# Optimization experiments

Hardware: AMD Instinct MI355X
Metric: run time of the kernel (lower is better)

## Reference

```python
import jax, jax.numpy as jnp
import numpy as np

DIM = 1024
HEADS = 16
DIM_HEAD = 64
NB_FEATURES = 266
EPS = 1e-4


def _gaussian_orthogonal_random_matrix(nb_rows, nb_cols, seed=0):
    # Blocks of orthogonal rows (QR of gaussian), rows rescaled by gaussian row norms (scaling=0).
    rng = np.random.default_rng(seed)
    blocks = []
    full, rem = divmod(nb_rows, nb_cols)
    for _ in range(full):
        g = rng.standard_normal((nb_cols, nb_cols))
        q, _ = np.linalg.qr(g)
        blocks.append(q.T)
    if rem > 0:
        g = rng.standard_normal((nb_cols, nb_cols))
        q, _ = np.linalg.qr(g)
        blocks.append(q.T[:rem])
    mat = np.concatenate(blocks, axis=0)
    multiplier = np.linalg.norm(rng.standard_normal((nb_rows, nb_cols)), axis=1)
    return (multiplier[:, None] * mat).astype(np.float32)


def _softmax_kernel(data, proj, is_query):
    # data: [b,h,n,d], proj: [m,d]
    d = data.shape[-1]
    data_normalizer = d ** -0.25
    ratio = proj.shape[0] ** -0.5
    data_dash = jnp.einsum('bhnd,md->bhnm', data * data_normalizer, proj)
    diag = 0.5 * (data_normalizer ** 2) * jnp.sum(data * data, axis=-1, keepdims=True)
    if is_query:
        m = jax.lax.stop_gradient(jnp.max(data_dash, axis=-1, keepdims=True))
    else:
        m = jax.lax.stop_gradient(jnp.max(data_dash, axis=(-1, -2), keepdims=True))
    return ratio * (jnp.exp(data_dash - diag - m) + EPS)


def _linear_attention(q, k, v):
    # q,k: [b,h,n,m], v: [b,h,n,e]
    k_cumsum = jnp.sum(k, axis=-2)                                   # [b,h,m]
    D_inv = 1.0 / jnp.einsum('bhnm,bhm->bhn', q, k_cumsum)           # [b,h,n]
    context = jnp.einsum('bhnm,bhne->bhme', k, v)                    # [b,h,m,e]
    return jnp.einsum('bhme,bhnm,bhn->bhne', context, q, D_inv)      # [b,h,n,e]


def setup_inputs() -> dict:
    key = jax.random.key(0)
    k1, k2, k3, k4, k5 = jax.random.split(key, 5)
    B, N = 2, 4096
    inner = HEADS * DIM_HEAD
    s = DIM ** -0.5
    return {
        'x': jax.random.normal(k1, (B, N, DIM), dtype=jnp.float32),
        'Wq': jax.random.normal(k2, (inner, DIM), dtype=jnp.float32) * s,
        'Wk': jax.random.normal(k3, (inner, DIM), dtype=jnp.float32) * s,
        'Wv': jax.random.normal(k4, (inner, DIM), dtype=jnp.float32) * s,
        'Wo': jax.random.normal(k5, (DIM, inner), dtype=jnp.float32) * s,
        'bo': jnp.zeros((DIM,), dtype=jnp.float32),
        'proj': jnp.asarray(_gaussian_orthogonal_random_matrix(NB_FEATURES, DIM_HEAD)),
    }


def reference(x, Wq, Wk, Wv, Wo, bo, proj):
    b, n, _ = x.shape
    def split_heads(t):
        return t.reshape(b, n, HEADS, DIM_HEAD).transpose(0, 2, 1, 3)  # [b,h,n,d]
    q = split_heads(x @ Wq.T)
    k = split_heads(x @ Wk.T)
    v = split_heads(x @ Wv.T)
    qp = _softmax_kernel(q, proj, is_query=True)
    kp = _softmax_kernel(k, proj, is_query=False)
    out = _linear_attention(qp, kp, v)                                # [b,h,n,d]
    out = out.transpose(0, 2, 1, 3).reshape(b, n, HEADS * DIM_HEAD)
    return out @ Wo.T + bo
```

## Files before the change

kernel.cpp:

```cpp
#include <hip/hip_runtime.h>
#include <hip/hip_bf16.h>
#include <hip/hip_fp16.h>


#define B_   2
#define N_   4096
#define H_   16
#define M_   266
#define MP_  288
#define DIM_ 1024
#define RT_  8192
#define BH_  32
#define LKN  40
#define LSB  296
#define NCH  16
#define KS_  8

typedef __attribute__((ext_vector_type(8))) short s8v;
typedef __attribute__((ext_vector_type(4))) float f4v;

__device__ __forceinline__ ushort f2bu(float x){ __hip_bfloat16 h = __float2bfloat16(x); return *(ushort*)&h; }

constexpr float NORMC  = 0.35355339059327379f;
constexpr float RATIOC = 0.06131393f;
constexpr float DIAGC  = 0.0625f;
constexpr float EPSC   = 1e-4f;

__device__ __forceinline__ unsigned encf(float x){
    unsigned b = __float_as_uint(x);
    return (b & 0x80000000u) ? ~b : (b | 0x80000000u);
}
__device__ __forceinline__ float decf(unsigned u){
    unsigned b = (u & 0x80000000u) ? (u ^ 0x80000000u) : ~u;
    return __uint_as_float(b);
}

__device__ __forceinline__ void stf(float* p, float v){ *p = v; }
__device__ __forceinline__ void stf(__hip_bfloat16* p, float v){ *p = __float2bfloat16(v); }

__device__ __forceinline__ void gl_lds16(const ushort* g, ushort* l){
    __builtin_amdgcn_global_load_lds(
        (const __attribute__((address_space(1))) unsigned int*)(const unsigned int*)g,
        (__attribute__((address_space(3))) unsigned int*)(unsigned int*)l,
        16, 0, 0);
}

__global__ void cast_x(const float* __restrict__ s, ushort* __restrict__ d){
    const int i = (blockIdx.x * 256 + threadIdx.x) * 8;
    const float4 a = *(const float4*)&s[i];
    const float4 b = *(const float4*)&s[i + 4];
    ushort4 lo, hi;
    lo.x = f2bu(a.x); lo.y = f2bu(a.y); lo.z = f2bu(a.z); lo.w = f2bu(a.w);
    hi.x = f2bu(b.x); hi.y = f2bu(b.y); hi.z = f2bu(b.z); hi.w = f2bu(b.w);
    *(ushort4*)&d[i]     = lo;
    *(ushort4*)&d[i + 4] = hi;
}

__global__ void cast_w(const float* s0, const float* s1, const float* s2, const float* s3,
                       ushort* d0, ushort* d1, ushort* d2, ushort* d3){
    const float* s; ushort* d;
    switch (blockIdx.y) {
        case 0: s = s0; d = d0; break;
        case 1: s = s1; d = d1; break;
        case 2: s = s2; d = d2; break;
        default: s = s3; d = d3; break;
    }
    const int i = (blockIdx.x * 256 + threadIdx.x) * 8;
    const float4 a = *(const float4*)&s[i];
    const float4 b = *(const float4*)&s[i + 4];
    ushort4 lo, hi;
    lo.x = f2bu(a.x); lo.y = f2bu(a.y); lo.z = f2bu(a.z); lo.w = f2bu(a.w);
    hi.x = f2bu(b.x); hi.y = f2bu(b.y); hi.z = f2bu(b.z); hi.w = f2bu(b.w);
    *(ushort4*)&d[i]     = lo;
    *(ushort4*)&d[i + 4] = hi;
}

__global__ void cast_proj(const float* __restrict__ p, ushort* __restrict__ pb){
    const int i = blockIdx.x * 256 + threadIdx.x;
    if (i >= MP_ * 64) return;
    const int m = i >> 6, dc = i & 63;
    pb[i] = f2bu((m < M_) ? NORMC * p[m * 64 + dc] : 0.f);
}

template<bool DIAG, bool BIAS, typename TC>
__launch_bounds__(256)
__global__ void gemm128(const ushort* __restrict__ A, const ushort* __restrict__ Bw,
                        const float* __restrict__ bias, TC* __restrict__ C,
                        float* __restrict__ diag)
{
    __shared__ ushort As[128 * 32];
    __shared__ ushort Bs[128 * 32];

    const int tid  = threadIdx.x;
    const int lane = tid & 63, wave = tid >> 6;
    const int col  = lane & 15, quad = lane >> 4;
    const int wm   = (wave & 1) * 64, wn = (wave >> 1) * 64;
    const int r0   = blockIdx.y * 128, c0 = blockIdx.x * 128;

    const int f0 = tid * 8;
    const int row0 = f0 >> 5, kc0 = f0 & 31;
    const size_t aoff0 = (size_t)(r0 + row0) * DIM_ + kc0;
    const size_t aoff1 = (size_t)(r0 + 64 + row0) * DIM_ + kc0;
    const size_t boff0 = (size_t)(c0 + row0) * DIM_ + kc0;
    const size_t boff1 = (size_t)(c0 + 64 + row0) * DIM_ + kc0;
    ushort* asb0 = &As[wave * 512];
    ushort* asb1 = &As[2048 + wave * 512];
    ushort* bsb0 = &Bs[wave * 512];
    ushort* bsb1 = &Bs[2048 + wave * 512];

    f4v acc[4][4];
    #pragma unroll
    for (int i = 0; i < 4; ++i)
        #pragma unroll
        for (int j = 0; j < 4; ++j) acc[i][j] = (f4v){0.f, 0.f, 0.f, 0.f};

    for (int kk = 0; kk < DIM_; kk += 32) {
        gl_lds16(&A[aoff0 + kk],  asb0);
        gl_lds16(&A[aoff1 + kk],  asb1);
        gl_lds16(&Bw[boff0 + kk], bsb0);
        gl_lds16(&Bw[boff1 + kk], bsb1);
        __syncthreads();
        s8v af[4], bf[4];
        #pragma unroll
        for (int i = 0; i < 4; ++i)
            af[i] = *(const s8v*)&As[(wm + i * 16 + col) * 32 + quad * 8];
        #pragma unroll
        for (int j = 0; j < 4; ++j)
            bf[j] = *(const s8v*)&Bs[(wn + j * 16 + col) * 32 + quad * 8];
        #pragma unroll
        for (int i = 0; i < 4; ++i)
            #pragma unroll
            for (int j = 0; j < 4; ++j)
                acc[i][j] = __builtin_amdgcn_mfma_f32_16x16x32_bf16(af[i], bf[j], acc[i][j], 0, 0, 0);
        __syncthreads();
    }

    float bb[4] = {0.f, 0.f, 0.f, 0.f};
    if (BIAS) {
        #pragma unroll
        for (int j = 0; j < 4; ++j) bb[j] = bias[c0 + wn + j * 16 + col];
    }
    #pragma unroll
    for (int i = 0; i < 4; ++i) {
        #pragma unroll
        for (int r = 0; r < 4; ++r) {
            const size_t grow = (size_t)(r0 + wm + i * 16 + quad * 4 + r);
            #pragma unroll
            for (int j = 0; j < 4; ++j)
                stf(&C[grow * DIM_ + c0 + wn + j * 16 + col], acc[i][j][r] + bb[j]);
        }
    }
    if (DIAG) {
        const int hglob = (c0 + wn) >> 6;
        #pragma unroll
        for (int i = 0; i < 4; ++i) {
            #pragma unroll
            for (int r = 0; r < 4; ++r) {
                float s = 0.f;
                #pragma unroll
                for (int j = 0; j < 4; ++j) s += acc[i][j][r] * acc[i][j][r];
                s += __shfl_xor(s, 1); s += __shfl_xor(s, 2);
                s += __shfl_xor(s, 4); s += __shfl_xor(s, 8);
                if (col == 0)
                    diag[(size_t)(r0 + wm + i * 16 + quad * 4 + r) * H_ + hglob] = DIAGC * s;
            }
        }
    }
}

__launch_bounds__(256)
__global__ void gemm128_qkv(const ushort* __restrict__ A, const ushort* __restrict__ Bw,
                            ushort* __restrict__ Q, ushort* __restrict__ K,
                            ushort* __restrict__ V,
                            float* __restrict__ diagQ, float* __restrict__ diagK)
{
    __shared__ ushort As[128 * 32];
    __shared__ ushort Bs[128 * 32];

    const int tid  = threadIdx.x;
    const int lane = tid & 63, wave = tid >> 6;
    const int col  = lane & 15, quad = lane >> 4;
    const int wm   = (wave & 1) * 64, wn = (wave >> 1) * 64;
    const int r0   = blockIdx.y * 128, c0 = blockIdx.x * 128;

    const int f0 = tid * 8;
    const int row0 = f0 >> 5, kc0 = f0 & 31;
    const size_t aoff0 = (size_t)(r0 + row0) * DIM_ + kc0;
    const size_t aoff1 = (size_t)(r0 + 64 + row0) * DIM_ + kc0;
    const size_t boff0 = (size_t)(c0 + row0) * DIM_ + kc0;
    const size_t boff1 = (size_t)(c0 + 64 + row0) * DIM_ + kc0;
    ushort* asb0 = &As[wave * 512];
    ushort* asb1 = &As[2048 + wave * 512];
    ushort* bsb0 = &Bs[wave * 512];
    ushort* bsb1 = &Bs[2048 + wave * 512];

    f4v acc[4][4];
    #pragma unroll
    for (int i = 0; i < 4; ++i)
        #pragma unroll
        for (int j = 0; j < 4; ++j) acc[i][j] = (f4v){0.f, 0.f, 0.f, 0.f};

    for (int kk = 0; kk < DIM_; kk += 32) {
        gl_lds16(&A[aoff0 + kk],  asb0);
        gl_lds16(&A[aoff1 + kk],  asb1);
        gl_lds16(&Bw[boff0 + kk], bsb0);
        gl_lds16(&Bw[boff1 + kk], bsb1);
        __syncthreads();
        s8v af[4], bf[4];
        #pragma unroll
        for (int i = 0; i < 4; ++i)
            af[i] = *(const s8v*)&As[(wm + i * 16 + col) * 32 + quad * 8];
        #pragma unroll
        for (int j = 0; j < 4; ++j)
            bf[j] = *(const s8v*)&Bs[(wn + j * 16 + col) * 32 + quad * 8];
        #pragma unroll
        for (int i = 0; i < 4; ++i)
            #pragma unroll
            for (int j = 0; j < 4; ++j)
                acc[i][j] = __builtin_amdgcn_mfma_f32_16x16x32_bf16(af[i], bf[j], acc[i][j], 0, 0, 0);
        __syncthreads();
    }

    const int which = c0 >> 10;
    const int cc    = c0 & 1023;
    ushort* C = (which == 0) ? Q : ((which == 1) ? K : V);
    float* dptr = (which == 0) ? diagQ : ((which == 1) ? diagK : nullptr);

    #pragma unroll
    for (int i = 0; i < 4; ++i) {
        #pragma unroll
        for (int r = 0; r < 4; ++r) {
            const size_t grow = (size_t)(r0 + wm + i * 16 + quad * 4 + r);
            #pragma unroll
            for (int j = 0; j < 4; ++j)
                C[grow * DIM_ + cc + wn + j * 16 + col] = f2bu(acc[i][j][r]);
        }
    }
    if (dptr) {
        const int hglob = (cc + wn) >> 6;
        #pragma unroll
        for (int i = 0; i < 4; ++i) {
            #pragma unroll
            for (int r = 0; r < 4; ++r) {
                float s = 0.f;
                #pragma unroll
                for (int j = 0; j < 4; ++j) s += acc[i][j][r] * acc[i][j][r];
                s += __shfl_xor(s, 1); s += __shfl_xor(s, 2);
                s += __shfl_xor(s, 4); s += __shfl_xor(s, 8);
                if (col == 0)
                    dptr[(size_t)(r0 + wm + i * 16 + quad * 4 + r) * H_ + hglob] = DIAGC * s;
            }
        }
    }
}

__launch_bounds__(256)
__global__ void kmax_mfma(const ushort* __restrict__ Kb, const ushort* __restrict__ projb,
                          unsigned* __restrict__ kmaxb)
{
    __shared__ ushort Pl[MP_ * 64];
    __shared__ float wmx[4];
    const int tid  = threadIdx.x;
    const int lane = tid & 63, wave = tid >> 6;
    const int col  = lane & 15, quad = lane >> 4;
    const int bh   = blockIdx.y, b = bh >> 4, h = bh & 15;

    const size_t arowB = ((size_t)(b * N_ + blockIdx.x * 256 + wave * 16 + col)) * DIM_ + h * 64 + quad * 8;
    s8v aP0 = *(const s8v*)&Kb[arowB];
    s8v aP1 = *(const s8v*)&Kb[arowB + 32];

    for (int i = tid; i < MP_ * 8; i += 256) {
        const int m = i >> 3, c = i & 7;
        *(uint4*)&Pl[m * 64 + ((c ^ (m & 7)) << 3)] = *(const uint4*)&projb[m * 64 + (c << 3)];
    }
    __syncthreads();

    const int sw0 = (quad ^ (col & 7)) << 3;
    const int sw1 = ((quad | 4) ^ (col & 7)) << 3;

    float mx = -3.4e38f;
    #pragma unroll
    for (int ni = 0; ni < 4; ++ni) {
        const s8v af0 = aP0, af1 = aP1;
        if (ni < 3) {
            aP0 = *(const s8v*)&Kb[arowB + (size_t)(ni + 1) * 64 * DIM_];
            aP1 = *(const s8v*)&Kb[arowB + (size_t)(ni + 1) * 64 * DIM_ + 32];
        }
        #pragma unroll
        for (int t = 0; t < 17; ++t) {
            const s8v bf0 = *(const s8v*)&Pl[(t * 16 + col) * 64 + sw0];
            const s8v bf1 = *(const s8v*)&Pl[(t * 16 + col) * 64 + sw1];
            f4v a = (f4v){0.f, 0.f, 0.f, 0.f};
            a = __builtin_amdgcn_mfma_f32_16x16x32_bf16(af0, bf0, a, 0, 0, 0);
            a = __builtin_amdgcn_mfma_f32_16x16x32_bf16(af1, bf1, a, 0, 0, 0);
            if (t * 16 + col < M_) {
                #pragma unroll
                for (int r = 0; r < 4; ++r) mx = fmaxf(mx, a[r]);
            }
        }
    }
    #pragma unroll
    for (int o = 32; o > 0; o >>= 1) mx = fmaxf(mx, __shfl_xor(mx, o));
    if (lane == 0) wmx[wave] = mx;
    __syncthreads();
    if (tid == 0)
        atomicMax(&kmaxb[bh], encf(fmaxf(fmaxf(wmx[0], wmx[1]), fmaxf(wmx[2], wmx[3]))));
}

__launch_bounds__(256)
__global__ void kctx_mfma(const ushort* __restrict__ Kb, const ushort* __restrict__ Vb,
                          const ushort* __restrict__ projb,
                          const float* __restrict__ diagK, const unsigned* __restrict__ kmaxb,
                          float* __restrict__ ctxp, float* __restrict__ kcsp)
{
    __shared__ ushort Pl[MP_ * 64];
    __shared__ ushort Kp[MP_ * LKN];
    __shared__ ushort Vt[64 * LKN];
    __shared__ float kred[2][MP_];

    const int tid  = threadIdx.x;
    const int lane = tid & 63, wave = tid >> 6;
    const int col  = lane & 15, quad = lane >> 4;
    const int bh   = blockIdx.y, b = bh >> 4, h = bh & 15;
    const int n0   = blockIdx.x * (N_ / NCH);
    const float kmax = decf(kmaxb[bh]);
    const int rowblk = wave >> 1;
    const int t0 = (wave & 1) * 9;

    const int nst = tid & 31, est = (tid >> 5) * 8;
    s8v vvP = *(const s8v*)&Vb[((size_t)(b * N_ + n0 + nst)) * DIM_ + h * 64 + est];
    const size_t arow0 = ((size_t)(b * N_ + n0 + rowblk * 16 + col)) * DIM_ + h * 64 + quad * 8;
    s8v afP0 = *(const s8v*)&Kb[arow0];
    s8v afP1 = *(const s8v*)&Kb[arow0 + 32];
    float dgrP[4];
    #pragma unroll
    for (int r = 0; r < 4; ++r)
        dgrP[r] = diagK[((size_t)(b * N_ + n0 + rowblk * 16 + quad * 4 + r)) * H_ + h];

    for (int i = tid; i < MP_ * 8; i += 256) {
        const int m = i >> 3, c = i & 7;
        *(uint4*)&Pl[m * 64 + ((c ^ (m & 7)) << 3)] = *(const uint4*)&projb[m * 64 + (c << 3)];
    }
    const int sw0 = (quad ^ (col & 7)) << 3;
    const int sw1 = ((quad | 4) ^ (col & 7)) << 3;

    f4v facc[18];
    #pragma unroll
    for (int t = 0; t < 18; ++t) facc[t] = (f4v){0.f, 0.f, 0.f, 0.f};
    float kcsa[9] = {};

    __syncthreads();

    for (int ks = 0; ks < KS_; ++ks) {
        const s8v vv = vvP, af0 = afP0, af1 = afP1;
        float dgr[4];
        #pragma unroll
        for (int r = 0; r < 4; ++r) dgr[r] = dgrP[r];

        #pragma unroll
        for (int j = 0; j < 8; ++j) Vt[(est + j) * LKN + nst] = ((const ushort*)&vv)[j];

        for (int t = t0; t < t0 + 9; ++t) {
            const s8v bf0 = *(const s8v*)&Pl[(t * 16 + col) * 64 + sw0];
            const s8v bf1 = *(const s8v*)&Pl[(t * 16 + col) * 64 + sw1];
            f4v a = (f4v){0.f, 0.f, 0.f, 0.f};
            a = __builtin_amdgcn_mfma_f32_16x16x32_bf16(af0, bf0, a, 0, 0, 0);
            a = __builtin_amdgcn_mfma_f32_16x16x32_bf16(af1, bf1, a, 0, 0, 0);
            const int m = t * 16 + col;
            float kp[4];
            #pragma unroll
            for (int r = 0; r < 4; ++r) {
                float v = 0.f;
                if (m < M_) v = RATIOC * (__expf(a[r] - dgr[r] - kmax) + EPSC);
                kp[r] = v;
            }
            kcsa[t - t0] += kp[0] + kp[1] + kp[2] + kp[3];
            ushort4 pk;
            pk.x = f2bu(kp[0]); pk.y = f2bu(kp[1]); pk.z = f2bu(kp[2]); pk.w = f2bu(kp[3]);
            *(ushort4*)&Kp[m * LKN + rowblk * 16 + quad * 4] = pk;
        }

        if (ks + 1 < KS_) {
            const int nb1 = n0 + (ks + 1) * 32;
            vvP  = *(const s8v*)&Vb[((size_t)(b * N_ + nb1 + nst)) * DIM_ + h * 64 + est];
            const size_t arow1 = ((size_t)(b * N_ + nb1 + rowblk * 16 + col)) * DIM_ + h * 64 + quad * 8;
            afP0 = *(const s8v*)&Kb[arow1];
            afP1 = *(const s8v*)&Kb[arow1 + 32];
            #pragma unroll
            for (int r = 0; r < 4; ++r)
                dgrP[r] = diagK[((size_t)(b * N_ + nb1 + rowblk * 16 + quad * 4 + r)) * H_ + h];
        }
        __syncthreads();
        const s8v bfe = *(const s8v*)&Vt[(wave * 16 + col) * LKN + quad * 8];
        #pragma unroll
        for (int t = 0; t < 18; ++t) {
            const s8v am = *(const s8v*)&Kp[(t * 16 + col) * LKN + quad * 8];
            facc[t] = __builtin_amdgcn_mfma_f32_16x16x32_bf16(am, bfe, facc[t], 0, 0, 0);
        }
        __syncthreads();
    }

    const size_t pbase = ((size_t)bh * NCH + blockIdx.x) * (MP_ * 64);
    #pragma unroll
    for (int t = 0; t < 18; ++t) {
        #pragma unroll
        for (int r = 0; r < 4; ++r)
            ctxp[pbase + (size_t)(t * 16 + quad * 4 + r) * 64 + wave * 16 + col] = facc[t][r];
    }
    for (int t = t0; t < t0 + 9; ++t) {
        float s = kcsa[t - t0];
        s += __shfl_xor(s, 16);
        s += __shfl_xor(s, 32);
        if (quad == 0) kred[rowblk][t * 16 + col] = s;
    }
    __syncthreads();
    for (int i = tid; i < MP_; i += 256)
        kcsp[((size_t)bh * NCH + blockIdx.x) * MP_ + i] = kred[0][i] + kred[1][i];
}

__launch_bounds__(256)
__global__ void ctx_reduce(const float* __restrict__ ctxp, const float* __restrict__ kcsp,
                           ushort* __restrict__ ctxT, float* __restrict__ kcs)
{
    const int bh = blockIdx.y, tid = threadIdx.x;
    const int base = blockIdx.x * (MP_ * 64 / 8);
    const size_t cb = (size_t)bh * NCH * (MP_ * 64);
    #pragma unroll
    for (int u = 0; u < 9; ++u) {
        const int flat = base + u * 256 + tid;
        float s = 0.f;
        #pragma unroll
        for (int c = 0; c < NCH; ++c) s += ctxp[cb + (size_t)c * (MP_ * 64) + flat];
        const int m = flat >> 6, e = flat & 63;
        ctxT[((size_t)bh * 64 + e) * MP_ + m] = f2bu(s);
    }
    if (blockIdx.x == 0) {
        for (int i = tid; i < MP_; i += 256) {
            float s = 0.f;
            #pragma unroll
            for (int c = 0; c < NCH; ++c) s += kcsp[((size_t)bh * NCH + c) * MP_ + i];
            kcs[(size_t)bh * MP_ + i] = s;
        }
    }
}

__launch_bounds__(256)
__global__ void qdashout(const ushort* __restrict__ Qb, const ushort* __restrict__ projb,
                         const float* __restrict__ diagQ, const float* __restrict__ kcs,
                         const ushort* __restrict__ ctxT, ushort* __restrict__ Ab)
{
    __shared__ ushort SB[64 * LSB];
    __shared__ float kcl[MP_];
    __shared__ float dinv[64];

    const int tid  = threadIdx.x;
    const int lane = tid & 63, wave = tid >> 6;
    const int col  = lane & 15, quad = lane >> 4;
    const int bh   = blockIdx.y, b = bh >> 4, h = bh & 15;
    const int n0   = blockIdx.x * 64;

    const size_t arow = ((size_t)(b * N_ + n0 + wave * 16 + col)) * DIM_ + h * 64 + quad * 8;
    const s8v af0 = *(const s8v*)&Qb[arow];
    const s8v af1 = *(const s8v*)&Qb[arow + 32];
    float dgr[4];
    #pragma unroll
    for (int r = 0; r < 4; ++r)
        dgr[r] = diagQ[((size_t)(b * N_ + n0 + wave * 16 + quad * 4 + r)) * H_ + h];

    for (int i = tid; i < MP_ * 8; i += 256) {
        const int m = i >> 3, c = i & 7;
        *(uint4*)&SB[m * 64 + ((c ^ (m & 7)) << 3)] = *(const uint4*)&projb[m * 64 + (c << 3)];
    }
    for (int i = tid; i < MP_; i += 256) kcl[i] = kcs[(size_t)bh * MP_ + i];
    __syncthreads();

    const int sw0 = (quad ^ (col & 7)) << 3;
    const int sw1 = ((quad | 4) ^ (col & 7)) << 3;

    f4v acc[17];
    #pragma unroll
    for (int t = 0; t < 17; ++t) {
        const s8v bf0 = *(const s8v*)&SB[(t * 16 + col) * 64 + sw0];
        const s8v bf1 = *(const s8v*)&SB[(t * 16 + col) * 64 + sw1];
        f4v a = (f4v){0.f, 0.f, 0.f, 0.f};
        a = __builtin_amdgcn_mfma_f32_16x16x32_bf16(af0, bf0, a, 0, 0, 0);
        a = __builtin_amdgcn_mfma_f32_16x16x32_bf16(af1, bf1, a, 0, 0, 0);
        acc[t] = a;
    }

    float rmx[4];
    #pragma unroll
    for (int r = 0; r < 4; ++r) {
        float mx = -3.4e38f;
        #pragma unroll
        for (int t = 0; t < 16; ++t) mx = fmaxf(mx, acc[t][r]);
        if (col < 10) mx = fmaxf(mx, acc[16][r]);
        mx = fmaxf(mx, __shfl_xor(mx, 1));
        mx = fmaxf(mx, __shfl_xor(mx, 2));
        mx = fmaxf(mx, __shfl_xor(mx, 4));
        mx = fmaxf(mx, __shfl_xor(mx, 8));
        rmx[r] = mx;
    }

    float den[4] = {0.f, 0.f, 0.f, 0.f};
    #pragma unroll
    for (int t = 0; t < 17; ++t) {
        const int m = t * 16 + col;
        const float kc = kcl[m];
        #pragma unroll
        for (int r = 0; r < 4; ++r) {
            float v = 0.f;
            if (m < M_)
                v = RATIOC * (__expf(acc[t][r] - dgr[r] - rmx[r]) + EPSC);
            acc[t][r] = v;
            den[r] += v * kc;
        }
    }

    const ushort* ct = ctxT + (size_t)bh * 64 * MP_;
    s8v bfA[4], bfB[4];
    #pragma unroll
    for (int j = 0; j < 4; ++j)
        bfA[j] = *(const s8v*)&ct[(size_t)(j * 16 + col) * MP_ + quad * 8];

    __syncthreads();

    #pragma unroll
    for (int r = 0; r < 4; ++r) {
        const int rb = (wave * 16 + quad * 4 + r) * LSB;
        #pragma unroll
        for (int t = 0; t < 17; ++t)
            SB[rb + t * 16 + col] = f2bu(acc[t][r]);
        if (col < 8) *(uint*)&SB[rb + 272 + col * 2] = 0u;
    }
    #pragma unroll
    for (int r = 0; r < 4; ++r) {
        float d = den[r];
        d += __shfl_xor(d, 1); d += __shfl_xor(d, 2);
        d += __shfl_xor(d, 4); d += __shfl_xor(d, 8);
        if (col == 0)
            dinv[wave * 16 + quad * 4 + r] = 1.0f / fmaxf(d, 1e-30f);
    }
    __syncthreads();

    f4v acc2[4];
    #pragma unroll
    for (int j = 0; j < 4; ++j) acc2[j] = (f4v){0.f, 0.f, 0.f, 0.f};
    #pragma unroll
    for (int kp = 0; kp < 4; ++kp) {
        const int k0 = 2 * kp, k1 = 2 * kp + 1, k2 = 2 * kp + 2;
        #pragma unroll
        for (int j = 0; j < 4; ++j)
            bfB[j] = *(const s8v*)&ct[(size_t)(j * 16 + col) * MP_ + k1 * 32 + quad * 8];
        const s8v afrA = *(const s8v*)&SB[(wave * 16 + col) * LSB + k0 * 32 + quad * 8];
        #pragma unroll
        for (int j = 0; j < 4; ++j)
            acc2[j] = __builtin_amdgcn_mfma_f32_16x16x32_bf16(afrA, bfA[j], acc2[j], 0, 0, 0);
        #pragma unroll
        for (int j = 0; j < 4; ++j)
            bfA[j] = *(const s8v*)&ct[(size_t)(j * 16 + col) * MP_ + k2 * 32 + quad * 8];
        const s8v afrB = *(const s8v*)&SB[(wave * 16 + col) * LSB + k1 * 32 + quad * 8];
        #pragma unroll
        for (int j = 0; j < 4; ++j)
            acc2[j] = __builtin_amdgcn_mfma_f32_16x16x32_bf16(afrB, bfB[j], acc2[j], 0, 0, 0);
    }
    {
        const s8v afrT = *(const s8v*)&SB[(wave * 16 + col) * LSB + 8 * 32 + quad * 8];
        #pragma unroll
        for (int j = 0; j < 4; ++j)
            acc2[j] = __builtin_amdgcn_mfma_f32_16x16x32_bf16(afrT, bfA[j], acc2[j], 0, 0, 0);
    }
    #pragma unroll
    for (int j = 0; j < 4; ++j) {
        #pragma unroll
        for (int r = 0; r < 4; ++r) {
            const int n = wave * 16 + quad * 4 + r;
            Ab[((size_t)(b * N_ + n0 + n)) * DIM_ + h * 64 + j * 16 + col] =
                f2bu(acc2[j][r] * dinv[n]);
        }
    }
}

extern "C" void kernel_launch(void* const* d_in, const int* in_sizes, int n_in,
                              void* d_out, int out_size, void* d_ws, size_t ws_size,
                              hipStream_t stream)
{
    const float* x    = (const float*)d_in[0];
    const float* Wq   = (const float*)d_in[1];
    const float* Wk   = (const float*)d_in[2];
    const float* Wv   = (const float*)d_in[3];
    const float* Wo   = (const float*)d_in[4];
    const float* bo   = (const float*)d_in[5];
    const float* proj = (const float*)d_in[6];

    char* ws = (char*)d_ws;
    size_t o = 0;
    ushort* xb    = (ushort*)(ws + o); o += (size_t)RT_ * DIM_ * 2;
    ushort* Wqb   = (ushort*)(ws + o); o += (size_t)DIM_ * DIM_ * 2;
    ushort* Wkb   = (ushort*)(ws + o); o += (size_t)DIM_ * DIM_ * 2;
    ushort* Wvb   = (ushort*)(ws + o); o += (size_t)DIM_ * DIM_ * 2;
    ushort* Wob   = (ushort*)(ws + o); o += (size_t)DIM_ * DIM_ * 2;
    ushort* projb = (ushort*)(ws + o); o += (size_t)MP_ * 64 * 2;
    ushort* Qb    = (ushort*)(ws + o); o += (size_t)RT_ * DIM_ * 2;
    ushort* Kb    = (ushort*)(ws + o); o += (size_t)RT_ * DIM_ * 2;
    ushort* Vb    = (ushort*)(ws + o); o += (size_t)RT_ * DIM_ * 2;
    ushort* Ab    = (ushort*)(ws + o); o += (size_t)RT_ * DIM_ * 2;
    float*    ctxp  = (float*)(ws + o);    o += (size_t)BH_ * NCH * MP_ * 64 * 4;
    float*    kcsp  = (float*)(ws + o);    o += (size_t)BH_ * NCH * MP_ * 4;
    float*    kcs   = (float*)(ws + o);    o += (size_t)BH_ * MP_ * 4;
    unsigned* kmaxb = (unsigned*)(ws + o); o += 128;
    float*    diagQ = (float*)(ws + o);    o += (size_t)RT_ * H_ * 4;
    float*    diagK = (float*)(ws + o);    o += (size_t)RT_ * H_ * 4;
    ushort*   ctxT  = (ushort*)(ws + o);   o += (size_t)BH_ * 64 * MP_ * 2;

    hipMemsetAsync(kmaxb, 0, 128, stream);

    cast_x<<<dim3(RT_ * DIM_ / 2048), 256, 0, stream>>>(x, xb);
    cast_w<<<dim3(DIM_ * DIM_ / 2048, 4), 256, 0, stream>>>(Wq, Wk, Wv, Wo, Wqb, Wkb, Wvb, Wob);
    cast_proj<<<dim3(MP_ * 64 / 256), 256, 0, stream>>>(proj, projb);

    gemm128_qkv<<<dim3(24, RT_ / 128), 256, 0, stream>>>(xb, Wqb, Qb, Kb, Vb, diagQ, diagK);

    kmax_mfma<<<dim3(16, BH_), 256, 0, stream>>>(Kb, projb, kmaxb);
    kctx_mfma<<<dim3(NCH, BH_), 256, 0, stream>>>(Kb, Vb, projb, diagK, kmaxb, ctxp, kcsp);
    ctx_reduce<<<dim3(8, BH_), 256, 0, stream>>>(ctxp, kcsp, ctxT, kcs);
    qdashout<<<dim3(N_ / 64, BH_), 256, 0, stream>>>(Qb, projb, diagQ, kcs, ctxT, Ab);

    gemm128<false, true, float><<<dim3(DIM_ / 128, RT_ / 128), 256, 0, stream>>>(Ab, Wob, bo, (float*)d_out, nullptr);
}
```

Baseline: 296.2 us.

## Fuse key max into context kernel with per-chunk rescaling; swizzle GEMM block order

Removes the separate kmax pass by having each context chunk compute its own local max and exponentiate against it. The reduction kernel then rescales each chunk's partial context and key sums by exp(local max minus global max), and adds the epsilon term analytically using column sums of V and N. The two GEMMs also remap block indices so consecutive blocks are spread across groups of eight, aiming for better L2 reuse. The cost is a second MFMA pass over K inside kctx and a little extra reduction work, in exchange for dropping one kernel launch, the memset and the atomic.

```diff
diff --git a/kernel.cpp b/kernel.cpp
--- a/kernel.cpp
+++ b/kernel.cpp
@@ -20,20 +20,12 @@
 typedef __attribute__((ext_vector_type(4))) float f4v;
 
 __device__ __forceinline__ ushort f2bu(float x){ __hip_bfloat16 h = __float2bfloat16(x); return *(ushort*)&h; }
+__device__ __forceinline__ float  bu2f(ushort u){ return __uint_as_float(((unsigned)u) << 16); }
 
 constexpr float NORMC  = 0.35355339059327379f;
 constexpr float RATIOC = 0.06131393f;
 constexpr float DIAGC  = 0.0625f;
 constexpr float EPSC   = 1e-4f;
-
-__device__ __forceinline__ unsigned encf(float x){
-    unsigned b = __float_as_uint(x);
-    return (b & 0x80000000u) ? ~b : (b | 0x80000000u);
-}
-__device__ __forceinline__ float decf(unsigned u){
-    unsigned b = (u & 0x80000000u) ? (u ^ 0x80000000u) : ~u;
-    return __uint_as_float(b);
-}
 
 __device__ __forceinline__ void stf(float* p, float v){ *p = v; }
 __device__ __forceinline__ void stf(__hip_bfloat16* p, float v){ *p = __float2bfloat16(v); }
@@ -95,7 +87,11 @@
     const int lane = tid & 63, wave = tid >> 6;
     const int col  = lane & 15, quad = lane >> 4;
     const int wm   = (wave & 1) * 64, wn = (wave >> 1) * 64;
-    const int r0   = blockIdx.y * 128, c0 = blockIdx.x * 128;
+
+    const int gX = gridDim.x, total = gX * gridDim.y, cpx = total >> 3;
+    const int fl = blockIdx.x + blockIdx.y * gX;
+    const int sw = (fl & 7) * cpx + (fl >> 3);
+    const int r0 = (sw / gX) * 128, c0 = (sw % gX) * 128;
 
     const int f0 = tid * 8;
     const int row0 = f0 >> 5, kc0 = f0 & 31;
@@ -181,7 +177,10 @@
     const int lane = tid & 63, wave = tid >> 6;
     const int col  = lane & 15, quad = lane >> 4;
     const int wm   = (wave & 1) * 64, wn = (wave >> 1) * 64;
-    const int r0   = blockIdx.y * 128, c0 = blockIdx.x * 128;
+
+    const int fl = blockIdx.x + blockIdx.y * 24;
+    const int sw = (fl & 7) * 192 + (fl >> 3);
+    const int r0 = (sw / 24) * 128, c0 = (sw % 24) * 128;
 
     const int f0 = tid * 8;
     const int row0 = f0 >> 5, kc0 = f0 & 31;
@@ -255,77 +254,65 @@
 }
 
 __launch_bounds__(256)
-__global__ void kmax_mfma(const ushort* __restrict__ Kb, const ushort* __restrict__ projb,
-                          unsigned* __restrict__ kmaxb)
-{
-    __shared__ ushort Pl[MP_ * 64];
-    __shared__ float wmx[4];
-    const int tid  = threadIdx.x;
-    const int lane = tid & 63, wave = tid >> 6;
-    const int col  = lane & 15, quad = lane >> 4;
-    const int bh   = blockIdx.y, b = bh >> 4, h = bh & 15;
-
-    const size_t arowB = ((size_t)(b * N_ + blockIdx.x * 256 + wave * 16 + col)) * DIM_ + h * 64 + quad * 8;
-    s8v aP0 = *(const s8v*)&Kb[arowB];
-    s8v aP1 = *(const s8v*)&Kb[arowB + 32];
-
-    for (int i = tid; i < MP_ * 8; i += 256) {
-        const int m = i >> 3, c = i & 7;
-        *(uint4*)&Pl[m * 64 + ((c ^ (m & 7)) << 3)] = *(const uint4*)&projb[m * 64 + (c << 3)];
-    }
-    __syncthreads();
-
-    const int sw0 = (quad ^ (col & 7)) << 3;
-    const int sw1 = ((quad | 4) ^ (col & 7)) << 3;
-
-    float mx = -3.4e38f;
-    #pragma unroll
-    for (int ni = 0; ni < 4; ++ni) {
-        const s8v af0 = aP0, af1 = aP1;
-        if (ni < 3) {
-            aP0 = *(const s8v*)&Kb[arowB + (size_t)(ni + 1) * 64 * DIM_];
-            aP1 = *(const s8v*)&Kb[arowB + (size_t)(ni + 1) * 64 * DIM_ + 32];
-        }
-        #pragma unroll
-        for (int t = 0; t < 17; ++t) {
-            const s8v bf0 = *(const s8v*)&Pl[(t * 16 + col) * 64 + sw0];
-            const s8v bf1 = *(const s8v*)&Pl[(t * 16 + col) * 64 + sw1];
-            f4v a = (f4v){0.f, 0.f, 0.f, 0.f};
-            a = __builtin_amdgcn_mfma_f32_16x16x32_bf16(af0, bf0, a, 0, 0, 0);
-            a = __builtin_amdgcn_mfma_f32_16x16x32_bf16(af1, bf1, a, 0, 0, 0);
-            if (t * 16 + col < M_) {
-                #pragma unroll
-                for (int r = 0; r < 4; ++r) mx = fmaxf(mx, a[r]);
-            }
-        }
-    }
-    #pragma unroll
-    for (int o = 32; o > 0; o >>= 1) mx = fmaxf(mx, __shfl_xor(mx, o));
-    if (lane == 0) wmx[wave] = mx;
-    __syncthreads();
-    if (tid == 0)
-        atomicMax(&kmaxb[bh], encf(fmaxf(fmaxf(wmx[0], wmx[1]), fmaxf(wmx[2], wmx[3]))));
-}
-
-__launch_bounds__(256)
 __global__ void kctx_mfma(const ushort* __restrict__ Kb, const ushort* __restrict__ Vb,
                           const ushort* __restrict__ projb,
-                          const float* __restrict__ diagK, const unsigned* __restrict__ kmaxb,
-                          float* __restrict__ ctxp, float* __restrict__ kcsp)
+                          const float* __restrict__ diagK,
+                          float* __restrict__ ctxp, float* __restrict__ kcsp,
+                          float* __restrict__ vsump, float* __restrict__ kmaxp)
 {
     __shared__ ushort Pl[MP_ * 64];
     __shared__ ushort Kp[MP_ * LKN];
     __shared__ ushort Vt[64 * LKN];
     __shared__ float kred[2][MP_];
+    __shared__ float wmx[4];
 
     const int tid  = threadIdx.x;
     const int lane = tid & 63, wave = tid >> 6;
     const int col  = lane & 15, quad = lane >> 4;
     const int bh   = blockIdx.y, b = bh >> 4, h = bh & 15;
     const int n0   = blockIdx.x * (N_ / NCH);
-    const float kmax = decf(kmaxb[bh]);
     const int rowblk = wave >> 1;
     const int t0 = (wave & 1) * 9;
+
+    for (int i = tid; i < MP_ * 8; i += 256) {
+        const int m = i >> 3, c = i & 7;
+        *(uint4*)&Pl[m * 64 + ((c ^ (m & 7)) << 3)] = *(const uint4*)&projb[m * 64 + (c << 3)];
+    }
+    const int sw0 = (quad ^ (col & 7)) << 3;
+    const int sw1 = ((quad | 4) ^ (col & 7)) << 3;
+    __syncthreads();
+
+    float mx = -3.4e38f;
+    {
+        size_t arA = ((size_t)(b * N_ + n0 + rowblk * 16 + col)) * DIM_ + h * 64 + quad * 8;
+        s8v pA0 = *(const s8v*)&Kb[arA];
+        s8v pA1 = *(const s8v*)&Kb[arA + 32];
+        for (int ks = 0; ks < KS_; ++ks) {
+            const s8v a0 = pA0, a1 = pA1;
+            if (ks + 1 < KS_) {
+                arA += (size_t)32 * DIM_;
+                pA0 = *(const s8v*)&Kb[arA];
+                pA1 = *(const s8v*)&Kb[arA + 32];
+            }
+            for (int t = t0; t < t0 + 9; ++t) {
+                const s8v bf0 = *(const s8v*)&Pl[(t * 16 + col) * 64 + sw0];
+                const s8v bf1 = *(const s8v*)&Pl[(t * 16 + col) * 64 + sw1];
+                f4v a = (f4v){0.f, 0.f, 0.f, 0.f};
+                a = __builtin_amdgcn_mfma_f32_16x16x32_bf16(a0, bf0, a, 0, 0, 0);
+                a = __builtin_amdgcn_mfma_f32_16x16x32_bf16(a1, bf1, a, 0, 0, 0);
+                if (t * 16 + col < M_) {
+                    #pragma unroll
+                    for (int r = 0; r < 4; ++r) mx = fmaxf(mx, a[r]);
+                }
+            }
+        }
+    }
+    #pragma unroll
+    for (int o = 32; o > 0; o >>= 1) mx = fmaxf(mx, __shfl_xor(mx, o));
+    if (lane == 0) wmx[wave] = mx;
+    __syncthreads();
+    const float mc = fmaxf(fmaxf(wmx[0], wmx[1]), fmaxf(wmx[2], wmx[3]));
+    if (tid == 0) kmaxp[bh * NCH + blockIdx.x] = mc;
 
     const int nst = tid & 31, est = (tid >> 5) * 8;
     s8v vvP = *(const s8v*)&Vb[((size_t)(b * N_ + n0 + nst)) * DIM_ + h * 64 + est];
@@ -337,19 +324,11 @@
     for (int r = 0; r < 4; ++r)
         dgrP[r] = diagK[((size_t)(b * N_ + n0 + rowblk * 16 + quad * 4 + r)) * H_ + h];
 
-    for (int i = tid; i < MP_ * 8; i += 256) {
-        const int m = i >> 3, c = i & 7;
-        *(uint4*)&Pl[m * 64 + ((c ^ (m & 7)) << 3)] = *(const uint4*)&projb[m * 64 + (c << 3)];
-    }
-    const int sw0 = (quad ^ (col & 7)) << 3;
-    const int sw1 = ((quad | 4) ^ (col & 7)) << 3;
-
     f4v facc[18];
     #pragma unroll
     for (int t = 0; t < 18; ++t) facc[t] = (f4v){0.f, 0.f, 0.f, 0.f};
     float kcsa[9] = {};
-
-    __syncthreads();
+    float vsa[8] = {};
 
     for (int ks = 0; ks < KS_; ++ks) {
         const s8v vv = vvP, af0 = afP0, af1 = afP1;
@@ -358,7 +337,11 @@
         for (int r = 0; r < 4; ++r) dgr[r] = dgrP[r];
 
         #pragma unroll
-        for (int j = 0; j < 8; ++j) Vt[(est + j) * LKN + nst] = ((const ushort*)&vv)[j];
+        for (int j = 0; j < 8; ++j) {
+            const ushort uv = ((const ushort*)&vv)[j];
+            Vt[(est + j) * LKN + nst] = uv;
+            vsa[j] += bu2f(uv);
+        }
 
         for (int t = t0; t < t0 + 9; ++t) {
             const s8v bf0 = *(const s8v*)&Pl[(t * 16 + col) * 64 + sw0];
@@ -371,7 +354,7 @@
             #pragma unroll
             for (int r = 0; r < 4; ++r) {
                 float v = 0.f;
-                if (m < M_) v = RATIOC * (__expf(a[r] - dgr[r] - kmax) + EPSC);
+                if (m < M_) v = __expf(a[r] - dgr[r] - mc);
                 kp[r] = v;
             }
             kcsa[t - t0] += kp[0] + kp[1] + kp[2] + kp[3];
@@ -407,6 +390,15 @@
         for (int r = 0; r < 4; ++r)
             ctxp[pbase + (size_t)(t * 16 + quad * 4 + r) * 64 + wave * 16 + col] = facc[t][r];
     }
+    #pragma unroll
+    for (int j = 0; j < 8; ++j) {
+        float s = vsa[j];
+        s += __shfl_xor(s, 1);  s += __shfl_xor(s, 2);
+        s += __shfl_xor(s, 4);  s += __shfl_xor(s, 8);
+        s += __shfl_xor(s, 16);
+        if ((lane & 31) == 0)
+            vsump[((size_t)bh * NCH + blockIdx.x) * 64 + est + j] = s;
+    }
     for (int t = t0; t < t0 + 9; ++t) {
         float s = kcsa[t - t0];
         s += __shfl_xor(s, 16);
@@ -420,9 +412,28 @@
 
 __launch_bounds__(256)
 __global__ void ctx_reduce(const float* __restrict__ ctxp, const float* __restrict__ kcsp,
+                           const float* __restrict__ vsump, const float* __restrict__ kmaxp,
                            ushort* __restrict__ ctxT, float* __restrict__ kcs)
 {
+    __shared__ float scl[NCH];
+    __shared__ float vsl[64];
     const int bh = blockIdx.y, tid = threadIdx.x;
+
+    if (tid < NCH) {
+        float M = -3.4e38f;
+        #pragma unroll
+        for (int c = 0; c < NCH; ++c) M = fmaxf(M, kmaxp[bh * NCH + c]);
+        scl[tid] = __expf(kmaxp[bh * NCH + tid] - M);
+    }
+    if (tid >= 64 && tid < 128) {
+        const int e = tid - 64;
+        float s = 0.f;
+        #pragma unroll
+        for (int c = 0; c < NCH; ++c) s += vsump[((size_t)bh * NCH + c) * 64 + e];
+        vsl[e] = s;
+    }
+    __syncthreads();
+
     const int base = blockIdx.x * (MP_ * 64 / 8);
     const size_t cb = (size_t)bh * NCH * (MP_ * 64);
     #pragma unroll
@@ -430,16 +441,16 @@
         const int flat = base + u * 256 + tid;
         float s = 0.f;
         #pragma unroll
-        for (int c = 0; c < NCH; ++c) s += ctxp[cb + (size_t)c * (MP_ * 64) + flat];
+        for (int c = 0; c < NCH; ++c) s += scl[c] * ctxp[cb + (size_t)c * (MP_ * 64) + flat];
         const int m = flat >> 6, e = flat & 63;
-        ctxT[((size_t)bh * 64 + e) * MP_ + m] = f2bu(s);
+        ctxT[((size_t)bh * 64 + e) * MP_ + m] = f2bu(RATIOC * (s + EPSC * vsl[e]));
     }
     if (blockIdx.x == 0) {
         for (int i = tid; i < MP_; i += 256) {
             float s = 0.f;
             #pragma unroll
-            for (int c = 0; c < NCH; ++c) s += kcsp[((size_t)bh * NCH + c) * MP_ + i];
-            kcs[(size_t)bh * MP_ + i] = s;
+            for (int c = 0; c < NCH; ++c) s += scl[c] * kcsp[((size_t)bh * NCH + c) * MP_ + i];
+            kcs[(size_t)bh * MP_ + i] = RATIOC * (s + EPSC * (float)N_);
         }
     }
 }
@@ -608,22 +619,20 @@
     float*    ctxp  = (float*)(ws + o);    o += (size_t)BH_ * NCH * MP_ * 64 * 4;
     float*    kcsp  = (float*)(ws + o);    o += (size_t)BH_ * NCH * MP_ * 4;
     float*    kcs   = (float*)(ws + o);    o += (size_t)BH_ * MP_ * 4;
-    unsigned* kmaxb = (unsigned*)(ws + o); o += 128;
+    float*    vsump = (float*)(ws + o);    o += (size_t)BH_ * NCH * 64 * 4;
+    float*    kmaxp = (float*)(ws + o);    o += (size_t)BH_ * NCH * 4;
     float*    diagQ = (float*)(ws + o);    o += (size_t)RT_ * H_ * 4;
     float*    diagK = (float*)(ws + o);    o += (size_t)RT_ * H_ * 4;
     ushort*   ctxT  = (ushort*)(ws + o);   o += (size_t)BH_ * 64 * MP_ * 2;
 
-    hipMemsetAsync(kmaxb, 0, 128, stream);
-
     cast_x<<<dim3(RT_ * DIM_ / 2048), 256, 0, stream>>>(x, xb);
     cast_w<<<dim3(DIM_ * DIM_ / 2048, 4), 256, 0, stream>>>(Wq, Wk, Wv, Wo, Wqb, Wkb, Wvb, Wob);
     cast_proj<<<dim3(MP_ * 64 / 256), 256, 0, stream>>>(proj, projb);
 
     gemm128_qkv<<<dim3(24, RT_ / 128), 256, 0, stream>>>(xb, Wqb, Qb, Kb, Vb, diagQ, diagK);
 
-    kmax_mfma<<<dim3(16, BH_), 256, 0, stream>>>(Kb, projb, kmaxb);
-    kctx_mfma<<<dim3(NCH, BH_), 256, 0, stream>>>(Kb, Vb, projb, diagK, kmaxb, ctxp, kcsp);
-    ctx_reduce<<<dim3(8, BH_), 256, 0, stream>>>(ctxp, kcsp, ctxT, kcs);
+    kctx_mfma<<<dim3(NCH, BH_), 256, 0, stream>>>(Kb, Vb, projb, diagK, ctxp, kcsp, vsump, kmaxp);
+    ctx_reduce<<<dim3(8, BH_), 256, 0, stream>>>(ctxp, kcsp, vsump, kmaxp, ctxT, kcs);
     qdashout<<<dim3(N_ / 64, BH_), 256, 0, stream>>>(Qb, projb, diagQ, kcs, ctxT, Ab);
 
     gemm128<false, true, float><<<dim3(DIM_ / 128, RT_ / 128), 256, 0, stream>>>(Ab, Wob, bo, (float*)d_out, nullptr);
```

Measured after the change: 278.5 us (median of 2 runs). 1.06x faster.
